# Performance work log

Hardware: AMD Instinct MI355X
Metric: run time of the kernel (lower is better)

Reference implementation:

```python
import jax, jax.numpy as jnp
import numpy as np

DT_REF = 1.0
EPS = 1e-5

def _ln(x, g, b):
    m = x.mean(-1, keepdims=True)
    v = ((x - m) ** 2).mean(-1, keepdims=True)
    return (x - m) * jax.lax.rsqrt(v + EPS) * g + b

def _conv(x, w):
    return jax.lax.conv_general_dilated(x, w, (1, 1), 'SAME', dimension_numbers=('NCHW', 'OIHW', 'NCHW'))

def _linscan(A, X):
    # h_t = A_t * h_{t-1} + X_t  via associative scan along axis=1 (time)
    def comb(c1, c2):
        a1, x1 = c1
        a2, x2 = c2
        return a1 * a2, x2 + a2 * x1
    return jax.lax.associative_scan(comb, (A, X), axis=1)[1]

def _forward(x_re, x_im, h_re, h_im, flux_re, flux_im, dt, gs_g, gs_b, wc_re, wc_im, bc_re, bc_im, metric, gt_g, gt_b, E_re, E_im, Einv_re, Einv_im, lam_flux, inj_re, inj_im, Wsrc_re, Wsrc_im, Wgate, bgate, lam_re, lam_im, Wg, W1, b1, W2, b2):
    B, T, D, H, W = x_re.shape
    x = jax.lax.complex(x_re, x_im)
    # ---- spatial: LayerNorm + Clifford (complex) conv scaled by Riemannian metric, residual ----
    xf = x.reshape(B * T, D, H, W)
    xr = jnp.concatenate([xf.real, xf.imag], axis=1)  # (N,2D,H,W)
    xn = _ln(xr.transpose(0, 2, 3, 1), gs_g, gs_b).transpose(0, 3, 1, 2)
    nr, ni = jnp.split(xn, 2, axis=1)
    o_re = (_conv(nr, wc_re) - _conv(ni, wc_im)) * metric + bc_re[None, :, None, None]
    o_im = (_conv(nr, wc_im) + _conv(ni, wc_re)) * metric + bc_im[None, :, None, None]
    x = (xf + jax.lax.complex(o_re, o_im)).reshape(B, T, D, H, W)
    # ---- eigenbasis encode ----
    E = jax.lax.complex(E_re, E_im)
    x_eigen = jnp.einsum('btdhw,de->bthwe', x, E)  # (B,T,H,W,D)
    x_mean = x_eigen.mean(axis=(2, 3))  # (B,T,D)
    dt_exp = jnp.broadcast_to(dt[None, :], (B, T))
    # ---- flux tracker: linear recurrence over T via pscan + carry-in correction ----
    A_flux = jnp.exp(-jax.nn.softplus(lam_flux)[None, None] * dt_exp[..., None] / DT_REF)  # (B,T,D) real
    X_flux = x_mean * jax.lax.complex(inj_re, inj_im)[None, None]
    flux_seq = _linscan(A_flux.astype(X_flux.dtype), X_flux)
    decay_cum = jnp.cumprod(A_flux, axis=1)
    flux_seq = flux_seq + jax.lax.complex(flux_re, flux_im)[:, None] * decay_cum
    source = jnp.einsum('btd,de->bte', flux_seq, jax.lax.complex(Wsrc_re, Wsrc_im))
    gate = jax.nn.sigmoid(flux_seq.real @ Wgate + bgate)  # (B,T,D) real in (0,1)
    g = gate[:, :, None, None, :]
    forcing = x_eigen * g + source[:, :, None, None, :] * (1.0 - g)
    # ---- ZOH transition operators ----
    lam = jax.lax.complex(-jax.nn.softplus(lam_re), lam_im)  # (D,) stable eigenvalues
    op_decay = jnp.exp(lam[None, None] * dt_exp[..., None])  # (B,T,D) complex
    op_forcing = (op_decay - 1.0) / lam
    u_t = forcing * op_forcing[:, :, None, None, :]
    h_prev = jax.lax.complex(h_re, h_im).reshape(B, H, W, D)
    u_t = u_t.at[:, 0].add(h_prev * op_decay[:, 0][:, None, None, :])
    A_full = jnp.broadcast_to(op_decay[:, :, None, None, :], u_t.shape)
    u_out = _linscan(A_full, u_t)  # state scan over T, independent per (b,h,w)
    # ---- decode + temporal LayerNorm + soft-MoE FFN residual ----
    x_dec = jnp.einsum('bthwe,ed->btdhw', u_out, jax.lax.complex(Einv_re, Einv_im))
    xr2 = jnp.concatenate([x_dec.real, x_dec.imag], axis=2).reshape(B * T, 2 * D, H, W)
    xn2 = _ln(xr2.transpose(0, 2, 3, 1), gt_g, gt_b)  # (N,H,W,2D)
    gates = jax.nn.softmax(xn2 @ Wg, axis=-1)  # (N,H,W,E)
    delta = jnp.zeros_like(xn2)
    for e in range(Wg.shape[-1]):  # small fixed expert count
        hdn = jax.nn.gelu(xn2 @ W1[e] + b1[e])
        delta = delta + gates[..., e:e + 1] * (hdn @ W2[e] + b2[e])
    y = xn2 + delta
    y_re, y_im = jnp.split(y, 2, axis=-1)
    x_out = jax.lax.complex(y_re, y_im).transpose(0, 3, 1, 2).reshape(B, T, D, H, W)
    z = x + x_out
    return jnp.concatenate([z.real, z.imag], axis=2)  # (B,T,2D,H,W) real view of complex out

def setup_inputs():
    B, T, D, H, W, E, F = 2, 16, 64, 48, 48, 4, 256
    key = jax.random.key(0)
    ks = jax.random.split(key, 32)
    n = lambda i, shape, s=1.0: jax.random.normal(ks[i], shape, dtype=jnp.float32) * s
    return {
        'x_re': n(0, (B, T, D, H, W)), 'x_im': n(1, (B, T, D, H, W)),
        'h_re': n(2, (B * H * W, 1, D)), 'h_im': n(3, (B * H * W, 1, D)),
        'flux_re': n(4, (B, D)), 'flux_im': n(5, (B, D)),
        'dt': jax.random.uniform(ks[6], (T,), dtype=jnp.float32, minval=0.1, maxval=1.0),
        'gs_g': jnp.ones((2 * D,), jnp.float32), 'gs_b': jnp.zeros((2 * D,), jnp.float32),
        'wc_re': n(7, (D, D, 3, 3), 0.02), 'wc_im': n(8, (D, D, 3, 3), 0.02),
        'bc_re': jnp.zeros((D,), jnp.float32), 'bc_im': jnp.zeros((D,), jnp.float32),
        'metric': jnp.ones((H, W), jnp.float32) + n(9, (H, W), 0.01),
        'gt_g': jnp.ones((2 * D,), jnp.float32), 'gt_b': jnp.zeros((2 * D,), jnp.float32),
        'E_re': n(10, (D, D), 0.125), 'E_im': n(11, (D, D), 0.125),
        'Einv_re': n(12, (D, D), 0.125), 'Einv_im': n(13, (D, D), 0.125),
        'lam_flux': n(14, (D,), 0.5),
        'inj_re': n(15, (D,), 0.1), 'inj_im': n(16, (D,), 0.1),
        'Wsrc_re': n(17, (D, D), 0.125), 'Wsrc_im': n(18, (D, D), 0.125),
        'Wgate': n(19, (D, D), 0.125), 'bgate': jnp.zeros((D,), jnp.float32),
        'lam_re': n(20, (D,), 0.5), 'lam_im': n(21, (D,), 0.5),
        'Wg': n(22, (2 * D, E), 0.1),
        'W1': n(23, (E, 2 * D, F), 0.06), 'b1': jnp.zeros((E, F), jnp.float32),
        'W2': n(24, (E, F, 2 * D), 0.04), 'b2': jnp.zeros((E, 2 * D), jnp.float32),
    }

def reference(x_re, x_im, h_re, h_im, flux_re, flux_im, dt, gs_g, gs_b, wc_re, wc_im, bc_re, bc_im, metric, gt_g, gt_b, E_re, E_im, Einv_re, Einv_im, lam_flux, inj_re, inj_im, Wsrc_re, Wsrc_im, Wgate, bgate, lam_re, lam_im, Wg, W1, b1, W2, b2):
    return _forward(x_re, x_im, h_re, h_im, flux_re, flux_im, dt, gs_g, gs_b, wc_re, wc_im, bc_re, bc_im, metric, gt_g, gt_b, E_re, E_im, Einv_re, Einv_im, lam_flux, inj_re, inj_im, Wsrc_re, Wsrc_im, Wgate, bgate, lam_re, lam_im, Wg, W1, b1, W2, b2)
```

## Files before the change

kernel.cpp:

```cpp
#include <hip/hip_runtime.h>
#include <hip/hip_bf16.h>
#include <math.h>

#define NBT 32
#define BB 2
#define TT 16
#define DD 64
#define CC 128
#define HH 48
#define WW2 48
#define HW 2304
#define NEXP 4
#define FF 256
#define EPS 1e-5f
#define PADROWS 2432

typedef __attribute__((ext_vector_type(8))) short bf16x8;
typedef __attribute__((ext_vector_type(4))) float f32x4;
typedef __attribute__((ext_vector_type(4))) unsigned int uint4v;
typedef __attribute__((ext_vector_type(2))) unsigned int uint2v;

static __device__ __forceinline__ unsigned short f2bf(float v) {
  __hip_bfloat16 h = __float2bfloat16(v);
  return *(unsigned short*)&h;
}

#define GLOAD_LDS16(gsrc, ldst) \
  __builtin_amdgcn_global_load_lds((const __attribute__((address_space(1))) unsigned int*)(gsrc), \
                                   (__attribute__((address_space(3))) unsigned int*)(ldst), 16, 0, 0)

__global__ void k_prep(unsigned int* __restrict__ xnb_u, float* __restrict__ xm,
                       const float* __restrict__ wc_re, const float* __restrict__ wc_im,
                       unsigned short* __restrict__ Wt,
                       const float* __restrict__ W1, const float* __restrict__ W2,
                       unsigned short* __restrict__ W1t, unsigned short* __restrict__ W2t,
                       const float* __restrict__ Einv_re, const float* __restrict__ Einv_im,
                       unsigned short* __restrict__ Bdt,
                       const float* __restrict__ E_re, const float* __restrict__ E_im,
                       unsigned short* __restrict__ Bet) {
  int blk = blockIdx.x;
  if (blk < 1024) {
    int u = blk * 256 + threadIdx.x;
    if (u < 4096) xm[u] = 0.f;
    if (u >= 32 * 128 * 64) return;
    int img = u >> 13;
    int rem = u & 8191;
    int row = rem >> 6;
    int cu  = rem & 63;
    int prow = row < 64 ? row : row + 2304;
    xnb_u[((size_t)img * PADROWS + prow) * 64 + cu] = 0u;
  } else if (blk < 1600) {
    int idx = (blk - 1024) * 256 + threadIdx.x;
    int tap = idx / 16384;
    int rem = idx & 16383;
    int cout = rem >> 7, cin = rem & 127;
    float v;
    if (cout < 64) {
      if (cin < 64) v =  wc_re[((size_t)cout * 64 + cin) * 9 + tap];
      else          v = -wc_im[((size_t)cout * 64 + (cin - 64)) * 9 + tap];
    } else {
      int o = cout - 64;
      if (cin < 64) v =  wc_im[((size_t)o * 64 + cin) * 9 + tap];
      else          v =  wc_re[((size_t)o * 64 + (cin - 64)) * 9 + tap];
    }
    Wt[idx] = f2bf(v);
  } else if (blk < 2112) {
    int idx = (blk - 1600) * 256 + threadIdx.x;
    {
      int e = idx >> 15, rem = idx & 32767, j = rem >> 7, k = rem & 127;
      float v = W1[((size_t)e * 128 + k) * 256 + j];
      int sw = ((((k >> 3) ^ (j & 7)) << 3) | (k & 7));
      W1t[(size_t)e * 32768 + j * 128 + sw] = f2bf(v);
    }
    {
      int e = idx >> 15, rem = idx & 32767, c = rem >> 8, k2 = rem & 255;
      float v = W2[((size_t)e * 256 + k2) * 128 + c];
      int sw = ((((k2 >> 3) ^ (c & 7)) << 3) | (k2 & 7));
      W2t[(size_t)e * 32768 + c * 256 + sw] = f2bf(v);
    }
  } else if (blk < 2176) {
    int idx = (blk - 2112) * 256 + threadIdx.x;
    int j = idx >> 7, k = idx & 127;
    float v;
    if (j < 64) {
      if (k < 64) v =  Einv_re[k * 64 + j];
      else        v = -Einv_im[(k - 64) * 64 + j];
    } else {
      int d = j - 64;
      if (k < 64) v =  Einv_im[k * 64 + d];
      else        v =  Einv_re[(k - 64) * 64 + d];
    }
    int sw = ((((k >> 3) ^ (j & 7)) << 3) | (k & 7));
    Bdt[j * 128 + sw] = f2bf(v);
  } else {
    int idx = (blk - 2176) * 256 + threadIdx.x;
    int j = idx >> 7, k = idx & 127;
    float v;
    if (j < 64) {
      if (k < 64) v =  E_re[k * 64 + j];
      else        v = -E_im[(k - 64) * 64 + j];
    } else {
      int d = j - 64;
      if (k < 64) v =  E_im[k * 64 + d];
      else        v =  E_re[(k - 64) * 64 + d];
    }
    int sw = ((((k >> 3) ^ (j & 7)) << 3) | (k & 7));
    Bet[j * 128 + sw] = f2bf(v);
  }
}

__global__ void k_ln1(const float* __restrict__ x_re, const float* __restrict__ x_im,
                      const float* __restrict__ g, const float* __restrict__ b,
                      unsigned short* __restrict__ xnb) {
  int n = blockIdx.x / 36;
  int hw0 = (blockIdx.x % 36) * 64;
  __shared__ float ls[64][129];
  __shared__ float part_s[4][64], part_q[4][64];
  __shared__ float mean_s[64], rstd_s[64];
  int tid = threadIdx.x;
  for (int i = tid; i < 64 * 128; i += 256) {
    int d = i >> 6, p = i & 63;
    float v = (d < DD) ? x_re[((size_t)n * DD + d) * HW + hw0 + p]
                       : x_im[((size_t)n * DD + (d - DD)) * HW + hw0 + p];
    ls[p][d] = v;
  }
  __syncthreads();
  {
    int p = tid & 63, q = tid >> 6;
    float s = 0.f, ss = 0.f;
    for (int c = q * 32; c < q * 32 + 32; c++) { float v = ls[p][c]; s += v; ss += v * v; }
    part_s[q][p] = s; part_q[q][p] = ss;
  }
  __syncthreads();
  if (tid < 64) {
    float s = part_s[0][tid] + part_s[1][tid] + part_s[2][tid] + part_s[3][tid];
    float ss = part_q[0][tid] + part_q[1][tid] + part_q[2][tid] + part_q[3][tid];
    float m = s * (1.f / CC);
    float var = ss * (1.f / CC) - m * m;
    mean_s[tid] = m; rstd_s[tid] = rsqrtf(var + EPS);
  }
  __syncthreads();
  for (int i = tid; i < 64 * 128; i += 256) {
    int p = i >> 7, c = i & 127;
    float v = (ls[p][c] - mean_s[p]) * rstd_s[p] * g[c] + b[c];
    xnb[(((size_t)n * PADROWS) + 64 + hw0 + p) * 128 + c] = f2bf(v);
  }
}

#define TM 128
#define AROWS 226

__global__ __launch_bounds__(512, 1) void k_conv(
    const unsigned short* __restrict__ xnb,
    const unsigned short* __restrict__ Wt,
    const float* __restrict__ bc_re, const float* __restrict__ bc_im,
    const float* __restrict__ metric,
    const float* __restrict__ x_re, const float* __restrict__ x_im,
    float* __restrict__ xp) {
  __shared__ unsigned short As[AROWS * 128];
  __shared__ unsigned short Bs[2][128 * 128];
  int n = blockIdx.x / 18;
  int tile = blockIdx.x % 18;
  int hw0 = tile * TM;
  int tid = threadIdx.x;
  int lane = tid & 63, wv = tid >> 6;
  int wvp = wv >> 1, wvc = wv & 1;
  int r16 = lane & 15, kgrp = lane >> 4;

  const unsigned short* xbase = xnb + ((size_t)n * PADROWS + 64 + hw0 - 49) * 128;
  for (int i = tid; i < AROWS * 16; i += 512) {
    int row = i >> 4, ch = i & 15;
    GLOAD_LDS16(xbase + (size_t)row * 128 + ((ch ^ (row & 7)) << 3), &As[i * 8]);
  }
  {
    #pragma unroll
    for (int it = 0; it < 4; it++) {
      int i = it * 512 + tid;
      int row = i >> 4, ch = i & 15;
      GLOAD_LDS16(Wt + (size_t)row * 128 + ((ch ^ (row & 7)) << 3), &Bs[0][i * 8]);
    }
  }

  f32x4 acc[2][4];
  #pragma unroll
  for (int am = 0; am < 2; am++)
    #pragma unroll
    for (int n0 = 0; n0 < 4; n0++) acc[am][n0] = (f32x4){0.f, 0.f, 0.f, 0.f};

  int w0 = (hw0 + wvp * 32 + r16) % 48;
  int w1 = (hw0 + wvp * 32 + 16 + r16) % 48;

  __syncthreads();

  for (int tap = 0; tap < 9; tap++) {
    int cur = tap & 1;
    if (tap < 8) {
      const unsigned short* wbase = Wt + (size_t)(tap + 1) * 16384;
      #pragma unroll
      for (int it = 0; it < 4; it++) {
        int i = it * 512 + tid;
        int row = i >> 4, ch = i & 15;
        GLOAD_LDS16(wbase + (size_t)row * 128 + ((ch ^ (row & 7)) << 3), &Bs[cur ^ 1][i * 8]);
      }
    }
    int ky = tap / 3, kx = tap % 3;
    int delta = (ky - 1) * 48 + (kx - 1);
    bool v0 = (unsigned)(w0 + kx - 1) < 48u;
    bool v1 = (unsigned)(w1 + kx - 1) < 48u;
    int lp0 = wvp * 32 + r16 + delta + 49;
    int lp1 = lp0 + 16;
    __builtin_amdgcn_s_setprio(1);
    #pragma unroll
    for (int k0 = 0; k0 < 4; k0++) {
      bf16x8 a0 = {0,0,0,0,0,0,0,0}, a1 = {0,0,0,0,0,0,0,0};
      if (v0) a0 = *(const bf16x8*)(As + lp0 * 128 + (((k0 * 4 + kgrp) ^ (lp0 & 7)) << 3));
      if (v1) a1 = *(const bf16x8*)(As + lp1 * 128 + (((k0 * 4 + kgrp) ^ (lp1 & 7)) << 3));
      #pragma unroll
      for (int n0 = 0; n0 < 4; n0++) {
        int brow = wvc * 64 + n0 * 16 + r16;
        bf16x8 b = *(const bf16x8*)(&Bs[cur][brow * 128 + (((k0 * 4 + kgrp) ^ (brow & 7)) << 3)]);
        acc[0][n0] = __builtin_amdgcn_mfma_f32_16x16x32_bf16(a0, b, acc[0][n0], 0, 0, 0);
        acc[1][n0] = __builtin_amdgcn_mfma_f32_16x16x32_bf16(a1, b, acc[1][n0], 0, 0, 0);
      }
    }
    __builtin_amdgcn_s_setprio(0);
    __syncthreads();
  }

  #pragma unroll
  for (int am = 0; am < 2; am++) {
    int prow0 = wvp * 32 + am * 16 + kgrp * 4;
    int pix0 = hw0 + prow0;
    f32x4 mets = *(const f32x4*)(metric + pix0);
    #pragma unroll
    for (int n0 = 0; n0 < 4; n0++) {
      int col = wvc * 64 + n0 * 16 + r16;
      float bias = (col < DD) ? bc_re[col] : bc_im[col - DD];
      const float* xsrc = (col < DD) ? (x_re + ((size_t)n * DD + col) * HW)
                                     : (x_im + ((size_t)n * DD + (col - DD)) * HW);
      f32x4 xres = *(const f32x4*)(xsrc + pix0);
      #pragma unroll
      for (int j = 0; j < 4; j++) {
        float v = acc[am][n0][j] * mets[j] + bias + xres[j];
        xp[((size_t)n * HW + pix0 + j) * 128 + col] = v;
      }
    }
  }
}

__global__ __launch_bounds__(256, 2) void k_eigen(
    const float* __restrict__ xp,
    const unsigned short* __restrict__ Bet,
    float* __restrict__ eg_re, float* __restrict__ eg_im,
    float* __restrict__ xm_re, float* __restrict__ xm_im) {
  __shared__ __attribute__((aligned(16))) unsigned char smem[81920];
  int tid = threadIdx.x;
  int blk = blockIdx.x;
  int n = blk / 36;
  size_t pos0 = (size_t)blk * 64;
  int lane = tid & 63, w = tid >> 6, wm = w >> 1, wn = w & 1;
  int r16 = lane & 15, kgrp = lane >> 4;

  unsigned short* BeL = (unsigned short*)smem;
  unsigned short* Axp = (unsigned short*)(smem + 32768);
  #pragma unroll
  for (int it = 0; it < 8; it++)
    GLOAD_LDS16(Bet + (size_t)(it * 256 + tid) * 8, &BeL[(it * 256 + tid) * 8]);
  #pragma unroll
  for (int it = 0; it < 8; it++) {
    int ci = it * 256 + tid;
    int p = ci >> 5, c4 = ci & 31;
    f32x4 v = *(const f32x4*)(xp + (pos0 + p) * 128 + c4 * 4);
    unsigned int lo = (unsigned int)f2bf(v[0]) | ((unsigned int)f2bf(v[1]) << 16);
    unsigned int hi = (unsigned int)f2bf(v[2]) | ((unsigned int)f2bf(v[3]) << 16);
    int chunk = c4 >> 1, sub = (c4 & 1) * 4;
    *(uint2v*)&Axp[p * 128 + ((chunk ^ (p & 7)) << 3) + sub] = (uint2v){lo, hi};
  }
  __syncthreads();
  f32x4 accD[2][4];
  #pragma unroll
  for (int mt = 0; mt < 2; mt++)
    #pragma unroll
    for (int nt = 0; nt < 4; nt++) accD[mt][nt] = (f32x4){0.f, 0.f, 0.f, 0.f};
  #pragma unroll
  for (int ks = 0; ks < 4; ks++) {
    int kc = ks * 4 + kgrp;
    bf16x8 a[2], bb[4];
    #pragma unroll
    for (int mt = 0; mt < 2; mt++) {
      int r = wm * 32 + mt * 16 + r16;
      a[mt] = *(const bf16x8*)&Axp[r * 128 + ((kc ^ (r & 7)) << 3)];
    }
    #pragma unroll
    for (int nt = 0; nt < 4; nt++) {
      int j = wn * 64 + nt * 16 + r16;
      bb[nt] = *(const bf16x8*)&BeL[j * 128 + ((kc ^ (j & 7)) << 3)];
    }
    #pragma unroll
    for (int mt = 0; mt < 2; mt++)
      #pragma unroll
      for (int nt = 0; nt < 4; nt++)
        accD[mt][nt] = __builtin_amdgcn_mfma_f32_16x16x32_bf16(a[mt], bb[nt], accD[mt][nt], 0, 0, 0);
  }
  __syncthreads();
  float* DsD = (float*)smem;
  #pragma unroll
  for (int mt = 0; mt < 2; mt++) {
    int row0 = wm * 32 + mt * 16 + kgrp * 4;
    #pragma unroll
    for (int nt = 0; nt < 4; nt++) {
      int c = wn * 64 + nt * 16 + r16;
      #pragma unroll
      for (int jj = 0; jj < 4; jj++)
        DsD[(row0 + jj) * 128 + c] = accD[mt][nt][jj];
    }
  }
  __syncthreads();
  float* red = (float*)(smem + 32768);
  int egq = tid & 15, pg = tid >> 4;
  int e0 = egq * 4;
  f32x4 psr = (f32x4){0.f,0.f,0.f,0.f}, psi = (f32x4){0.f,0.f,0.f,0.f};
  #pragma unroll
  for (int i = 0; i < 4; i++) {
    int p = pg + 16 * i;
    size_t pos = pos0 + p;
    f32x4 ar = *(const f32x4*)&DsD[p * 128 + e0];
    f32x4 ai = *(const f32x4*)&DsD[p * 128 + 64 + e0];
    *(f32x4*)&eg_re[pos * 64 + e0] = ar;
    *(f32x4*)&eg_im[pos * 64 + e0] = ai;
    psr += ar; psi += ai;
  }
  *(f32x4*)&red[pg * 64 + e0] = psr;
  *(f32x4*)&red[1024 + pg * 64 + e0] = psi;
  __syncthreads();
  if (tid < 128) {
    int e = tid & 63, which = tid >> 6;
    const float* rb = red + which * 1024;
    float s = 0.f;
    #pragma unroll
    for (int p = 0; p < 16; p++) s += rb[p * 64 + e];
    float* dst = which ? xm_im : xm_re;
    atomicAdd(&dst[n * DD + e], s * (1.f / HW));
  }
}

__global__ void k_seq1(const float* __restrict__ xm_re, const float* __restrict__ xm_im,
                       const float* __restrict__ dt, const float* __restrict__ lam_flux,
                       const float* __restrict__ inj_re, const float* __restrict__ inj_im,
                       const float* __restrict__ flux_re0, const float* __restrict__ flux_im0,
                       float* __restrict__ frg, float* __restrict__ fig) {
  int b = blockIdx.x;
  int e = threadIdx.x;
  float lx = lam_flux[e];
  float sp = lx > 20.f ? lx : log1pf(expf(lx));
  float f_r = flux_re0[b * DD + e], f_i = flux_im0[b * DD + e];
  float ij_r = inj_re[e], ij_i = inj_im[e];
  for (int t = 0; t < TT; t++) {
    float A = expf(-sp * dt[t]);
    int bt = b * TT + t;
    float xr = xm_re[bt * DD + e], xi = xm_im[bt * DD + e];
    f_r = A * f_r + (xr * ij_r - xi * ij_i);
    f_i = A * f_i + (xr * ij_i + xi * ij_r);
    frg[bt * DD + e] = f_r; fig[bt * DD + e] = f_i;
  }
}

__global__ void k_seq2(const float* __restrict__ frg, const float* __restrict__ fig,
                       const float* __restrict__ dt,
                       const float* __restrict__ Wsrc_re, const float* __restrict__ Wsrc_im,
                       const float* __restrict__ Wgate, const float* __restrict__ bgate,
                       const float* __restrict__ lam_re, const float* __restrict__ lam_im,
                       float* __restrict__ gate, float* __restrict__ src_re, float* __restrict__ src_im,
                       float* __restrict__ od_re, float* __restrict__ od_im,
                       float* __restrict__ of_re, float* __restrict__ of_im) {
  int bt = blockIdx.x;
  int t = bt % TT;
  int e = threadIdx.x;
  __shared__ float fr[DD], fi[DD];
  fr[e] = frg[bt * DD + e];
  fi[e] = fig[bt * DD + e];
  __syncthreads();
  float sr = 0.f, si = 0.f, gl = bgate[e];
  for (int d2 = 0; d2 < DD; d2++) {
    float r = fr[d2], im = fi[d2];
    float wr = Wsrc_re[d2 * DD + e], wi = Wsrc_im[d2 * DD + e];
    sr += r * wr - im * wi;
    si += r * wi + im * wr;
    gl += r * Wgate[d2 * DD + e];
  }
  src_re[bt * DD + e] = sr; src_im[bt * DD + e] = si;
  gate[bt * DD + e] = 1.f / (1.f + expf(-gl));
  float lre = lam_re[e];
  float lr_v = -(lre > 20.f ? lre : log1pf(expf(lre)));
  float li_v = lam_im[e];
  float den = lr_v * lr_v + li_v * li_v;
  float dtv = dt[t];
  float mag = expf(lr_v * dtv);
  float odr = mag * cosf(li_v * dtv);
  float odi = mag * sinf(li_v * dtv);
  od_re[bt * DD + e] = odr; od_im[bt * DD + e] = odi;
  of_re[bt * DD + e] = ((odr - 1.f) * lr_v + odi * li_v) / den;
  of_im[bt * DD + e] = (odi * lr_v - (odr - 1.f) * li_v) / den;
}

__global__ void k_uscan(float* __restrict__ eg_re, float* __restrict__ eg_im,
                        const float* __restrict__ gate,
                        const float* __restrict__ src_re, const float* __restrict__ src_im,
                        const float* __restrict__ od_re, const float* __restrict__ od_im,
                        const float* __restrict__ of_re, const float* __restrict__ of_im,
                        const float* __restrict__ h_re, const float* __restrict__ h_im) {
  size_t gid = (size_t)blockIdx.x * 256 + threadIdx.x;
  int e = (int)(gid & 63);
  size_t rem = gid >> 6;
  int hw = (int)(rem % HW);
  int b = (int)(rem / HW);
  float u_r = 0.f, u_i = 0.f;
  for (int t = 0; t < TT; t++) {
    int bt = b * TT + t;
    size_t idx = ((size_t)bt * HW + hw) * DD + e;
    float g = gate[bt * DD + e];
    float fr2 = eg_re[idx] * g + src_re[bt * DD + e] * (1.f - g);
    float fi2 = eg_im[idx] * g + src_im[bt * DD + e] * (1.f - g);
    float ofr = of_re[bt * DD + e], ofi = of_im[bt * DD + e];
    float ut_r = fr2 * ofr - fi2 * ofi;
    float ut_i = fr2 * ofi + fi2 * ofr;
    float odr = od_re[bt * DD + e], odi = od_im[bt * DD + e];
    if (t == 0) {
      size_t hidx = ((size_t)b * HW + hw) * DD + e;
      float hr = h_re[hidx], hi = h_im[hidx];
      ut_r += hr * odr - hi * odi;
      ut_i += hr * odi + hi * odr;
    }
    float nu_r = odr * u_r - odi * u_i + ut_r;
    float nu_i = odr * u_i + odi * u_r + ut_i;
    u_r = nu_r; u_i = nu_i;
    eg_re[idx] = u_r; eg_im[idx] = u_i;
  }
}

__global__ __launch_bounds__(256, 2) void k_dmoe(
    const float* u_re, const float* u_im,
    const unsigned short* __restrict__ Bdt,
    const float* __restrict__ Wg,
    float* __restrict__ gates,
    const float* __restrict__ xp,
    const unsigned short* __restrict__ W1t, const unsigned short* __restrict__ W2t,
    const float* __restrict__ b1, const float* __restrict__ b2,
    const float* __restrict__ gt_g, const float* __restrict__ gt_b,
    float* __restrict__ out) {
  __shared__ __attribute__((aligned(16))) unsigned char smem[81920];
  int tid = threadIdx.x;
  int blk = blockIdx.x;
  int n = blk / 36;
  int hw0 = (blk % 36) * 64;
  size_t pos0 = (size_t)blk * 64;
  int lane = tid & 63, w = tid >> 6, wm = w >> 1, wn = w & 1;
  int r16 = lane & 15, kgrp = lane >> 4;

  {
    unsigned short* BdL = (unsigned short*)smem;
    unsigned short* Au  = (unsigned short*)(smem + 32768);
    #pragma unroll
    for (int it = 0; it < 8; it++)
      GLOAD_LDS16(Bdt + (size_t)(it * 256 + tid) * 8, &BdL[(it * 256 + tid) * 8]);
    #pragma unroll
    for (int it = 0; it < 8; it++) {
      int ci = it * 256 + tid;
      int p = ci >> 5, c4 = ci & 31;
      f32x4 v;
      if (c4 < 16) v = *(const f32x4*)(u_re + (size_t)(pos0 + p) * 64 + c4 * 4);
      else         v = *(const f32x4*)(u_im + (size_t)(pos0 + p) * 64 + (c4 - 16) * 4);
      unsigned int lo = (unsigned int)f2bf(v[0]) | ((unsigned int)f2bf(v[1]) << 16);
      unsigned int hi = (unsigned int)f2bf(v[2]) | ((unsigned int)f2bf(v[3]) << 16);
      int chunk = c4 >> 1, sub = (c4 & 1) * 4;
      *(uint2v*)&Au[p * 128 + ((chunk ^ (p & 7)) << 3) + sub] = (uint2v){lo, hi};
    }
    __syncthreads();
    f32x4 accD[2][4];
    #pragma unroll
    for (int mt = 0; mt < 2; mt++)
      #pragma unroll
      for (int nt = 0; nt < 4; nt++) accD[mt][nt] = (f32x4){0.f, 0.f, 0.f, 0.f};
    #pragma unroll
    for (int ks = 0; ks < 4; ks++) {
      int kc = ks * 4 + kgrp;
      bf16x8 a[2], bb[4];
      #pragma unroll
      for (int mt = 0; mt < 2; mt++) {
        int r = wm * 32 + mt * 16 + r16;
        a[mt] = *(const bf16x8*)&Au[r * 128 + ((kc ^ (r & 7)) << 3)];
      }
      #pragma unroll
      for (int nt = 0; nt < 4; nt++) {
        int j = wn * 64 + nt * 16 + r16;
        bb[nt] = *(const bf16x8*)&BdL[j * 128 + ((kc ^ (j & 7)) << 3)];
      }
      #pragma unroll
      for (int mt = 0; mt < 2; mt++)
        #pragma unroll
        for (int nt = 0; nt < 4; nt++)
          accD[mt][nt] = __builtin_amdgcn_mfma_f32_16x16x32_bf16(a[mt], bb[nt], accD[mt][nt], 0, 0, 0);
    }
    __syncthreads();
    float* DsD = (float*)smem;
    #pragma unroll
    for (int mt = 0; mt < 2; mt++) {
      int row0 = wm * 32 + mt * 16 + kgrp * 4;
      #pragma unroll
      for (int nt = 0; nt < 4; nt++) {
        int c = wn * 64 + nt * 16 + r16;
        #pragma unroll
        for (int jj = 0; jj < 4; jj++)
          DsD[(row0 + jj) * 128 + c] = accD[mt][nt][jj];
      }
    }
    __syncthreads();
    float* Yl = (float*)(smem + 32768);
    unsigned short* Xb = (unsigned short*)(smem + 65536);
    int egq = tid & 15, pg = tid >> 4;
    int d0 = egq * 4, swz = pg & 7;
    f32x4 gg0 = *(const f32x4*)(gt_g + d0);
    f32x4 gb0 = *(const f32x4*)(gt_b + d0);
    f32x4 gg1 = *(const f32x4*)(gt_g + 64 + d0);
    f32x4 gb1 = *(const f32x4*)(gt_b + 64 + d0);
    f32x4 wgr[4], wgi[4];
    #pragma unroll
    for (int j = 0; j < 4; j++) {
      wgr[j] = *(const f32x4*)&Wg[(d0 + j) * 4];
      wgi[j] = *(const f32x4*)&Wg[(64 + d0 + j) * 4];
    }
    int cre = ((d0 >> 3) ^ swz) << 3;
    int cim = (((64 + d0) >> 3) ^ swz) << 3;
    int off47 = d0 & 7;
    #pragma unroll
    for (int i = 0; i < 4; i++) {
      int p = pg + 16 * i;
      size_t pos = pos0 + p;
      f32x4 acr = *(const f32x4*)&DsD[p * 128 + d0];
      f32x4 aci = *(const f32x4*)&DsD[p * 128 + 64 + d0];
      float s = acr[0] + acr[1] + acr[2] + acr[3]
              + aci[0] + aci[1] + aci[2] + aci[3];
      float q = acr[0]*acr[0] + acr[1]*acr[1] + acr[2]*acr[2] + acr[3]*acr[3]
              + aci[0]*aci[0] + aci[1]*aci[1] + aci[2]*aci[2] + aci[3]*aci[3];
      #pragma unroll
      for (int off = 8; off >= 1; off >>= 1) {
        s += __shfl_xor(s, off);
        q += __shfl_xor(q, off);
      }
      float mean = s * (1.f / CC);
      float rstd = rsqrtf(q * (1.f / CC) - mean * mean + EPS);
      f32x4 lnr = (acr - mean) * rstd * gg0 + gb0;
      f32x4 lni = (aci - mean) * rstd * gg1 + gb1;
      *(f32x4*)&Yl[p * 128 + d0] = lnr;
      *(f32x4*)&Yl[p * 128 + 64 + d0] = lni;
      f32x4 p4 = lnr[0]*wgr[0] + lnr[1]*wgr[1] + lnr[2]*wgr[2] + lnr[3]*wgr[3]
               + lni[0]*wgi[0] + lni[1]*wgi[1] + lni[2]*wgi[2] + lni[3]*wgi[3];
      float p0 = p4[0], p1 = p4[1], p2 = p4[2], p3 = p4[3];
      #pragma unroll
      for (int off = 8; off >= 1; off >>= 1) {
        p0 += __shfl_xor(p0, off); p1 += __shfl_xor(p1, off);
        p2 += __shfl_xor(p2, off); p3 += __shfl_xor(p3, off);
      }
      if (egq == 0) {
        float m = fmaxf(fmaxf(p0, p1), fmaxf(p2, p3));
        float e0v = __expf(p0 - m), e1v = __expf(p1 - m), e2v = __expf(p2 - m), e3v = __expf(p3 - m);
        float inv = 1.f / (e0v + e1v + e2v + e3v);
        f32x4 g4 = {e0v * inv, e1v * inv, e2v * inv, e3v * inv};
        *(f32x4*)(gates + pos * 4) = g4;
      }
      unsigned int r0 = (unsigned int)f2bf(lnr[0]) | ((unsigned int)f2bf(lnr[1]) << 16);
      unsigned int r1 = (unsigned int)f2bf(lnr[2]) | ((unsigned int)f2bf(lnr[3]) << 16);
      unsigned int i0 = (unsigned int)f2bf(lni[0]) | ((unsigned int)f2bf(lni[1]) << 16);
      unsigned int i1 = (unsigned int)f2bf(lni[2]) | ((unsigned int)f2bf(lni[3]) << 16);
      *(uint2v*)&Xb[p * 128 + cre + off47] = (uint2v){r0, r1};
      *(uint2v*)&Xb[p * 128 + cim + off47] = (uint2v){i0, i1};
    }
  }
  __syncthreads();

  unsigned short* W1s = (unsigned short*)smem;
  unsigned short* W2s = (unsigned short*)(smem + 32768);
  unsigned short* Hs  = (unsigned short*)(smem + 65536);
  float* Ds = (float*)smem;
  f32x4 acc2[2][4];
  {
    const float* YlF = (const float*)(smem + 32768);
    #pragma unroll
    for (int mt = 0; mt < 2; mt++) {
      int row0 = wm * 32 + mt * 16 + kgrp * 4;
      #pragma unroll
      for (int nt = 0; nt < 4; nt++) {
        int c = wn * 64 + nt * 16 + r16;
        #pragma unroll
        for (int jj = 0; jj < 4; jj++)
          acc2[mt][nt][jj] = YlF[(row0 + jj) * 128 + c];
      }
    }
  }
  bf16x8 xa[2][4];
  {
    const unsigned short* Xb = (const unsigned short*)(smem + 65536);
    #pragma unroll
    for (int pt = 0; pt < 2; pt++) {
      int r = wm * 32 + pt * 16 + r16;
      #pragma unroll
      for (int ks = 0; ks < 4; ks++) {
        int kc = ks * 4 + kgrp;
        xa[pt][ks] = *(const bf16x8*)&Xb[r * 128 + ((kc ^ (r & 7)) << 3)];
      }
    }
  }
  __syncthreads();
  {
    #pragma unroll
    for (int it = 0; it < 8; it++)
      GLOAD_LDS16(W1t + (size_t)(it * 256 + tid) * 8, &W1s[(it * 256 + tid) * 8]);
  }
  __syncthreads();

  const float c1 = -2.3022084f;
  const float c2 = -0.10294372f;

  for (int s = 0; s < 8; s++) {
    int e = s >> 1, h = s & 1;
    float grp[2];
    #pragma unroll
    for (int pt = 0; pt < 2; pt++)
      grp[pt] = gates[(pos0 + wm * 32 + pt * 16 + r16) * 4 + e];
    f32x4 b1p[4];
    #pragma unroll
    for (int ft = 0; ft < 4; ft++)
      b1p[ft] = *(const f32x4*)&b1[e * 256 + h * 128 + wn * 64 + ft * 16 + kgrp * 4];
    {
      const unsigned short* w2src = W2t + (size_t)e * 32768 + (size_t)h * 128;
      #pragma unroll
      for (int it = 0; it < 8; it++) {
        int i = it * 256 + tid;
        int c = i >> 4, j = i & 15;
        GLOAD_LDS16(w2src + (size_t)c * 256 + j * 8, &W2s[i * 8]);
      }
    }
    f32x4 acc1[4][2];
    #pragma unroll
    for (int ft = 0; ft < 4; ft++)
      #pragma unroll
      for (int pt = 0; pt < 2; pt++) acc1[ft][pt] = (f32x4){0.f, 0.f, 0.f, 0.f};
    __builtin_amdgcn_s_setprio(1);
    #pragma unroll
    for (int ks = 0; ks < 4; ks++) {
      int kc = ks * 4 + kgrp;
      bf16x8 wf[4];
      #pragma unroll
      for (int ft = 0; ft < 4; ft++) {
        int fr = wn * 64 + ft * 16 + r16;
        wf[ft] = *(const bf16x8*)&W1s[fr * 128 + ((kc ^ (fr & 7)) << 3)];
      }
      #pragma unroll
      for (int ft = 0; ft < 4; ft++)
        #pragma unroll
        for (int pt = 0; pt < 2; pt++)
          acc1[ft][pt] = __builtin_amdgcn_mfma_f32_16x16x32_bf16(wf[ft], xa[pt][ks], acc1[ft][pt], 0, 0, 0);
    }
    __builtin_amdgcn_s_setprio(0);
    #pragma unroll
    for (int ft = 0; ft < 4; ft++) {
      int f0 = wn * 64 + ft * 16 + kgrp * 4;
      int chunk = f0 >> 3, sub = f0 & 7;
      #pragma unroll
      for (int pt = 0; pt < 2; pt++) {
        int pl = wm * 32 + pt * 16 + r16;
        float gr = grp[pt];
        unsigned short hb[4];
        #pragma unroll
        for (int jj = 0; jj < 4; jj++) {
          float x = acc1[ft][pt][jj] + b1p[ft][jj];
          float z = x * (c1 + c2 * x * x);
          float t = __builtin_amdgcn_exp2f(z);
          hb[jj] = f2bf(x * gr * __builtin_amdgcn_rcpf(1.f + t));
        }
        unsigned int lo = (unsigned int)hb[0] | ((unsigned int)hb[1] << 16);
        unsigned int hi = (unsigned int)hb[2] | ((unsigned int)hb[3] << 16);
        *(uint2v*)&Hs[pl * 128 + ((chunk ^ (pl & 7)) << 3) + sub] = (uint2v){lo, hi};
      }
    }
    __syncthreads();
    if (s < 7) {
      int sn = s + 1;
      const unsigned short* w1src = W1t + (size_t)(sn >> 1) * 32768 + (size_t)(sn & 1) * 16384;
      #pragma unroll
      for (int it = 0; it < 8; it++)
        GLOAD_LDS16(w1src + (size_t)(it * 256 + tid) * 8, &W1s[(it * 256 + tid) * 8]);
    }
    __builtin_amdgcn_s_setprio(1);
    #pragma unroll
    for (int ks = 0; ks < 4; ks++) {
      int kc = ks * 4 + kgrp;
      bf16x8 a[2], bb[4];
      #pragma unroll
      for (int mt = 0; mt < 2; mt++) {
        int r = wm * 32 + mt * 16 + r16;
        a[mt] = *(const bf16x8*)&Hs[r * 128 + ((kc ^ (r & 7)) << 3)];
      }
      #pragma unroll
      for (int nt = 0; nt < 4; nt++) {
        int c = wn * 64 + nt * 16 + r16;
        bb[nt] = *(const bf16x8*)&W2s[c * 128 + ((kc ^ (c & 7)) << 3)];
      }
      #pragma unroll
      for (int mt = 0; mt < 2; mt++)
        #pragma unroll
        for (int nt = 0; nt < 4; nt++)
          acc2[mt][nt] = __builtin_amdgcn_mfma_f32_16x16x32_bf16(a[mt], bb[nt], acc2[mt][nt], 0, 0, 0);
    }
    __builtin_amdgcn_s_setprio(0);
    __syncthreads();
  }

  #pragma unroll
  for (int mt = 0; mt < 2; mt++) {
    int row0 = wm * 32 + mt * 16 + kgrp * 4;
    #pragma unroll
    for (int nt = 0; nt < 4; nt++) {
      int c = wn * 64 + nt * 16 + r16;
      #pragma unroll
      for (int jj = 0; jj < 4; jj++)
        Ds[(row0 + jj) * 129 + c] = acc2[mt][nt][jj];
    }
  }
  __syncthreads();
  #pragma unroll
  for (int it = 0; it < 8; it++) {
    int qi = it * 256 + tid;
    int p = qi >> 5, cq = (qi & 31) << 2;
    size_t pos = pos0 + p;
    f32x4 xpv = *(const f32x4*)&xp[pos * 128 + cq];
    f32x4 g4  = *(const f32x4*)&gates[pos * 4];
    f32x4 bt0 = *(const f32x4*)&b2[0 * CC + cq];
    f32x4 bt1 = *(const f32x4*)&b2[1 * CC + cq];
    f32x4 bt2 = *(const f32x4*)&b2[2 * CC + cq];
    f32x4 bt3 = *(const f32x4*)&b2[3 * CC + cq];
    int base = p * 129 + cq;
    #pragma unroll
    for (int j = 0; j < 4; j++) {
      float bterm = g4[0] * bt0[j] + g4[1] * bt1[j] + g4[2] * bt2[j] + g4[3] * bt3[j];
      Ds[base + j] = xpv[j] + Ds[base + j] + bterm;
    }
  }
  __syncthreads();
  {
    int p = tid & 63;
    int cg = tid >> 6;
    const float* Drow = Ds + p * 129;
    size_t obase = ((size_t)n * CC) * HW + hw0 + p;
    #pragma unroll
    for (int i = 0; i < 32; i++) {
      int c = i * 4 + cg;
      out[obase + (size_t)c * HW] = Drow[c];
    }
  }
}

extern "C" void kernel_launch(void* const* d_in, const int* in_sizes, int n_in,
                              void* d_out, int out_size, void* d_ws, size_t ws_size,
                              hipStream_t stream) {
  const float* x_re   = (const float*)d_in[0];
  const float* x_im   = (const float*)d_in[1];
  const float* h_re   = (const float*)d_in[2];
  const float* h_im   = (const float*)d_in[3];
  const float* flux_re= (const float*)d_in[4];
  const float* flux_im= (const float*)d_in[5];
  const float* dt     = (const float*)d_in[6];
  const float* gs_g   = (const float*)d_in[7];
  const float* gs_b   = (const float*)d_in[8];
  const float* wc_re  = (const float*)d_in[9];
  const float* wc_im  = (const float*)d_in[10];
  const float* bc_re  = (const float*)d_in[11];
  const float* bc_im  = (const float*)d_in[12];
  const float* metric = (const float*)d_in[13];
  const float* gt_g   = (const float*)d_in[14];
  const float* gt_b   = (const float*)d_in[15];
  const float* E_re   = (const float*)d_in[16];
  const float* E_im   = (const float*)d_in[17];
  const float* Einv_re= (const float*)d_in[18];
  const float* Einv_im= (const float*)d_in[19];
  const float* lam_flux=(const float*)d_in[20];
  const float* inj_re = (const float*)d_in[21];
  const float* inj_im = (const float*)d_in[22];
  const float* Wsrc_re= (const float*)d_in[23];
  const float* Wsrc_im= (const float*)d_in[24];
  const float* Wgate  = (const float*)d_in[25];
  const float* bgate  = (const float*)d_in[26];
  const float* lam_re = (const float*)d_in[27];
  const float* lam_im = (const float*)d_in[28];
  const float* Wg     = (const float*)d_in[29];
  const float* W1     = (const float*)d_in[30];
  const float* b1     = (const float*)d_in[31];
  const float* W2     = (const float*)d_in[32];
  const float* b2     = (const float*)d_in[33];

  float* ws = (float*)d_ws;
  const size_t SZ_FULL = (size_t)NBT * HW * CC;
  const size_t SZ_HALF = (size_t)NBT * HW * DD;
  float* xp    = ws;
  float* eg_re = xp + SZ_FULL;
  float* eg_im = eg_re + SZ_HALF;
  float* xr2   = eg_im + SZ_HALF;
  unsigned short* xnb = (unsigned short*)xr2;
  unsigned short* Wt  = (unsigned short*)(xr2 + 5000000);
  float* smalls = xr2 + SZ_FULL;
  float* xm_re = smalls;
  float* xm_im = xm_re + 2048;
  float* gatep = xm_im + 2048;
  float* src_re= gatep + 2048;
  float* src_im= src_re + 2048;
  float* od_re = src_im + 2048;
  float* od_im = od_re + 2048;
  float* of_re = od_im + 2048;
  float* of_im = of_re + 2048;
  float* gates = of_im + 2048;
  unsigned short* W1t = (unsigned short*)(gates + (size_t)NBT * HW * 4);
  unsigned short* W2t = W1t + 131072;
  float* frg = (float*)(W2t + 131072);
  float* fig = frg + 2048;
  unsigned short* Bdt = (unsigned short*)(fig + 2048);
  unsigned short* Bet = Bdt + 16384;

  hipLaunchKernelGGL(k_prep, dim3(2240), dim3(256), 0, stream,
                     (unsigned int*)xnb, xm_re, wc_re, wc_im, Wt, W1, W2, W1t, W2t,
                     Einv_re, Einv_im, Bdt, E_re, E_im, Bet);
  hipLaunchKernelGGL(k_ln1, dim3(NBT * 36), dim3(256), 0, stream, x_re, x_im, gs_g, gs_b, xnb);
  hipLaunchKernelGGL(k_conv, dim3(NBT * 18), dim3(512), 0, stream,
                     xnb, Wt, bc_re, bc_im, metric, x_re, x_im, xp);
  hipLaunchKernelGGL(k_eigen, dim3(1152), dim3(256), 0, stream,
                     xp, Bet, eg_re, eg_im, xm_re, xm_im);
  hipLaunchKernelGGL(k_seq1, dim3(BB), dim3(DD), 0, stream,
                     xm_re, xm_im, dt, lam_flux, inj_re, inj_im, flux_re, flux_im, frg, fig);
  hipLaunchKernelGGL(k_seq2, dim3(NBT), dim3(DD), 0, stream,
                     frg, fig, dt, Wsrc_re, Wsrc_im, Wgate, bgate, lam_re, lam_im,
                     gatep, src_re, src_im, od_re, od_im, of_re, of_im);
  hipLaunchKernelGGL(k_uscan, dim3(1152), dim3(256), 0, stream,
                     eg_re, eg_im, gatep, src_re, src_im, od_re, od_im, of_re, of_im, h_re, h_im);
  hipLaunchKernelGGL(k_dmoe, dim3(1152), dim3(256), 0, stream,
                     eg_re, eg_im, Bdt, Wg,
                     gates, xp, W1t, W2t, b1, b2, gt_g, gt_b,
                     (float*)d_out);
}
```

Measured before the change: 203.9 us.

## Fuse eigenbasis projection and spatial mean into the conv epilogue

```diff
diff --git a/kernel.cpp b/kernel.cpp
--- a/kernel.cpp
+++ b/kernel.cpp
@@ -156,7 +156,10 @@
     const float* __restrict__ bc_re, const float* __restrict__ bc_im,
     const float* __restrict__ metric,
     const float* __restrict__ x_re, const float* __restrict__ x_im,
-    float* __restrict__ xp) {
+    float* __restrict__ xp,
+    const unsigned short* __restrict__ Bet,
+    float* __restrict__ eg_re, float* __restrict__ eg_im,
+    float* __restrict__ xm_re, float* __restrict__ xm_im) {
   __shared__ unsigned short As[AROWS * 128];
   __shared__ unsigned short Bs[2][128 * 128];
   int n = blockIdx.x / 18;
@@ -227,6 +230,15 @@
     __syncthreads();
   }
 
+  {
+    #pragma unroll
+    for (int it = 0; it < 4; it++)
+      GLOAD_LDS16(Bet + (size_t)(it * 512 + tid) * 8, &As[(it * 512 + tid) * 8]);
+  }
+  float* red = (float*)&As[16384];
+  if (tid < 128) red[tid] = 0.f;
+
+  unsigned short* Xe = &Bs[0][0];
   #pragma unroll
   for (int am = 0; am < 2; am++) {
     int prow0 = wvp * 32 + am * 16 + kgrp * 4;
@@ -239,108 +251,71 @@
       const float* xsrc = (col < DD) ? (x_re + ((size_t)n * DD + col) * HW)
                                      : (x_im + ((size_t)n * DD + (col - DD)) * HW);
       f32x4 xres = *(const f32x4*)(xsrc + pix0);
+      int swc = ((col >> 3) << 3) | (col & 7);
       #pragma unroll
       for (int j = 0; j < 4; j++) {
         float v = acc[am][n0][j] * mets[j] + bias + xres[j];
         xp[((size_t)n * HW + pix0 + j) * 128 + col] = v;
-      }
-    }
-  }
-}
-
-__global__ __launch_bounds__(256, 2) void k_eigen(
-    const float* __restrict__ xp,
-    const unsigned short* __restrict__ Bet,
-    float* __restrict__ eg_re, float* __restrict__ eg_im,
-    float* __restrict__ xm_re, float* __restrict__ xm_im) {
-  __shared__ __attribute__((aligned(16))) unsigned char smem[81920];
-  int tid = threadIdx.x;
-  int blk = blockIdx.x;
-  int n = blk / 36;
-  size_t pos0 = (size_t)blk * 64;
-  int lane = tid & 63, w = tid >> 6, wm = w >> 1, wn = w & 1;
-  int r16 = lane & 15, kgrp = lane >> 4;
-
-  unsigned short* BeL = (unsigned short*)smem;
-  unsigned short* Axp = (unsigned short*)(smem + 32768);
-  #pragma unroll
-  for (int it = 0; it < 8; it++)
-    GLOAD_LDS16(Bet + (size_t)(it * 256 + tid) * 8, &BeL[(it * 256 + tid) * 8]);
-  #pragma unroll
-  for (int it = 0; it < 8; it++) {
-    int ci = it * 256 + tid;
-    int p = ci >> 5, c4 = ci & 31;
-    f32x4 v = *(const f32x4*)(xp + (pos0 + p) * 128 + c4 * 4);
-    unsigned int lo = (unsigned int)f2bf(v[0]) | ((unsigned int)f2bf(v[1]) << 16);
-    unsigned int hi = (unsigned int)f2bf(v[2]) | ((unsigned int)f2bf(v[3]) << 16);
-    int chunk = c4 >> 1, sub = (c4 & 1) * 4;
-    *(uint2v*)&Axp[p * 128 + ((chunk ^ (p & 7)) << 3) + sub] = (uint2v){lo, hi};
-  }
-  __syncthreads();
-  f32x4 accD[2][4];
-  #pragma unroll
-  for (int mt = 0; mt < 2; mt++)
-    #pragma unroll
-    for (int nt = 0; nt < 4; nt++) accD[mt][nt] = (f32x4){0.f, 0.f, 0.f, 0.f};
-  #pragma unroll
-  for (int ks = 0; ks < 4; ks++) {
-    int kc = ks * 4 + kgrp;
-    bf16x8 a[2], bb[4];
-    #pragma unroll
-    for (int mt = 0; mt < 2; mt++) {
-      int r = wm * 32 + mt * 16 + r16;
-      a[mt] = *(const bf16x8*)&Axp[r * 128 + ((kc ^ (r & 7)) << 3)];
+        int pix = prow0 + j;
+        Xe[pix * 128 + ((((col >> 3) ^ (pix & 7)) << 3) | (col & 7))] = f2bf(v);
+      }
+      (void)swc;
+    }
+  }
+  __syncthreads();
+
+  {
+    const unsigned short* BetL = (const unsigned short*)As;
+    int half = wv >> 2, wmE = (wv >> 1) & 1, wnE = wv & 1;
+    f32x4 accE[2][4];
+    #pragma unroll
+    for (int mt = 0; mt < 2; mt++)
+      #pragma unroll
+      for (int nt = 0; nt < 4; nt++) accE[mt][nt] = (f32x4){0.f, 0.f, 0.f, 0.f};
+    #pragma unroll
+    for (int ks = 0; ks < 4; ks++) {
+      int kc = ks * 4 + kgrp;
+      bf16x8 a[2], bb[4];
+      #pragma unroll
+      for (int mt = 0; mt < 2; mt++) {
+        int r = half * 64 + wmE * 32 + mt * 16 + r16;
+        a[mt] = *(const bf16x8*)&Xe[r * 128 + ((kc ^ (r & 7)) << 3)];
+      }
+      #pragma unroll
+      for (int nt = 0; nt < 4; nt++) {
+        int j = wnE * 64 + nt * 16 + r16;
+        bb[nt] = *(const bf16x8*)&BetL[j * 128 + ((kc ^ (j & 7)) << 3)];
+      }
+      #pragma unroll
+      for (int mt = 0; mt < 2; mt++)
+        #pragma unroll
+        for (int nt = 0; nt < 4; nt++)
+          accE[mt][nt] = __builtin_amdgcn_mfma_f32_16x16x32_bf16(a[mt], bb[nt], accE[mt][nt], 0, 0, 0);
     }
     #pragma unroll
     for (int nt = 0; nt < 4; nt++) {
-      int j = wn * 64 + nt * 16 + r16;
-      bb[nt] = *(const bf16x8*)&BeL[j * 128 + ((kc ^ (j & 7)) << 3)];
-    }
-    #pragma unroll
-    for (int mt = 0; mt < 2; mt++)
-      #pragma unroll
-      for (int nt = 0; nt < 4; nt++)
-        accD[mt][nt] = __builtin_amdgcn_mfma_f32_16x16x32_bf16(a[mt], bb[nt], accD[mt][nt], 0, 0, 0);
-  }
-  __syncthreads();
-  float* DsD = (float*)smem;
-  #pragma unroll
-  for (int mt = 0; mt < 2; mt++) {
-    int row0 = wm * 32 + mt * 16 + kgrp * 4;
-    #pragma unroll
-    for (int nt = 0; nt < 4; nt++) {
-      int c = wn * 64 + nt * 16 + r16;
-      #pragma unroll
-      for (int jj = 0; jj < 4; jj++)
-        DsD[(row0 + jj) * 128 + c] = accD[mt][nt][jj];
-    }
-  }
-  __syncthreads();
-  float* red = (float*)(smem + 32768);
-  int egq = tid & 15, pg = tid >> 4;
-  int e0 = egq * 4;
-  f32x4 psr = (f32x4){0.f,0.f,0.f,0.f}, psi = (f32x4){0.f,0.f,0.f,0.f};
-  #pragma unroll
-  for (int i = 0; i < 4; i++) {
-    int p = pg + 16 * i;
-    size_t pos = pos0 + p;
-    f32x4 ar = *(const f32x4*)&DsD[p * 128 + e0];
-    f32x4 ai = *(const f32x4*)&DsD[p * 128 + 64 + e0];
-    *(f32x4*)&eg_re[pos * 64 + e0] = ar;
-    *(f32x4*)&eg_im[pos * 64 + e0] = ai;
-    psr += ar; psi += ai;
-  }
-  *(f32x4*)&red[pg * 64 + e0] = psr;
-  *(f32x4*)&red[1024 + pg * 64 + e0] = psi;
+      int j2 = wnE * 64 + nt * 16 + r16;
+      float psum = 0.f;
+      #pragma unroll
+      for (int mt = 0; mt < 2; mt++) {
+        int row0 = half * 64 + wmE * 32 + mt * 16 + kgrp * 4;
+        #pragma unroll
+        for (int jj = 0; jj < 4; jj++) {
+          float v = accE[mt][nt][jj];
+          size_t pos = (size_t)n * HW + hw0 + row0 + jj;
+          if (j2 < 64) eg_re[pos * 64 + j2] = v;
+          else         eg_im[pos * 64 + (j2 - 64)] = v;
+          psum += v;
+        }
+      }
+      atomicAdd(&red[j2], psum);
+    }
+  }
   __syncthreads();
   if (tid < 128) {
-    int e = tid & 63, which = tid >> 6;
-    const float* rb = red + which * 1024;
-    float s = 0.f;
-    #pragma unroll
-    for (int p = 0; p < 16; p++) s += rb[p * 64 + e];
-    float* dst = which ? xm_im : xm_re;
-    atomicAdd(&dst[n * DD + e], s * (1.f / HW));
+    float val = red[tid] * (1.f / HW);
+    if (tid < 64) atomicAdd(&xm_re[n * DD + tid], val);
+    else          atomicAdd(&xm_im[n * DD + (tid - 64)], val);
   }
 }
 
@@ -830,9 +805,8 @@
                      Einv_re, Einv_im, Bdt, E_re, E_im, Bet);
   hipLaunchKernelGGL(k_ln1, dim3(NBT * 36), dim3(256), 0, stream, x_re, x_im, gs_g, gs_b, xnb);
   hipLaunchKernelGGL(k_conv, dim3(NBT * 18), dim3(512), 0, stream,
-                     xnb, Wt, bc_re, bc_im, metric, x_re, x_im, xp);
-  hipLaunchKernelGGL(k_eigen, dim3(1152), dim3(256), 0, stream,
-                     xp, Bet, eg_re, eg_im, xm_re, xm_im);
+                     xnb, Wt, bc_re, bc_im, metric, x_re, x_im, xp,
+                     Bet, eg_re, eg_im, xm_re, xm_im);
   hipLaunchKernelGGL(k_seq1, dim3(BB), dim3(DD), 0, stream,
                      xm_re, xm_im, dt, lam_flux, inj_re, inj_im, flux_re, flux_im, frg, fig);
   hipLaunchKernelGGL(k_seq2, dim3(NBT), dim3(DD), 0, stream,
```

New measurement: 201.0 us. No clear change (-1.4%).
